# Kernel optimization log

Measured on AMD Instinct MI355X. Metric: run time of the kernel, lower is better.

Reference implementation:

```python
import jax, jax.numpy as jnp
import numpy as np


def _gru_dir(x_seq, h0, w_ih, w_hh, b_ih, b_hh, reverse):
    """Single-direction GRU over time (PyTorch gate math, gate order r,z,n).
    x_seq: [T,B,I], h0: [B,H], w_ih: [3H,I], w_hh: [3H,H].
    Returns outputs [T,B,H] in original time order."""
    # Precompute input projections for all timesteps in one GEMM.
    gi = jnp.einsum('tbi,gi->tbg', x_seq, w_ih) + b_ih  # [T,B,3H]

    def step(h, gi_t):
        gh = h @ w_hh.T + b_hh                     # [B,3H]
        ir, iz, inn = jnp.split(gi_t, 3, axis=-1)
        hr, hz, hn = jnp.split(gh, 3, axis=-1)
        r = jax.nn.sigmoid(ir + hr)
        z = jax.nn.sigmoid(iz + hz)
        n = jnp.tanh(inn + r * hn)
        h_new = (1.0 - z) * n + z * h
        return h_new, h_new

    _, ys = jax.lax.scan(step, h0, gi, reverse=reverse)
    return ys


def setup_inputs() -> dict:
    key = jax.random.key(0)
    ks = jax.random.split(key, 6)
    T, B, I, H, L = 256, 64, 2048, 1024, 3
    s = 1.0 / np.sqrt(H)  # PyTorch-style init scale
    return {
        'x': jax.random.normal(ks[0], (T, B, I), jnp.float32),
        'h0': jax.random.normal(ks[1], (2 * L, B, H), jnp.float32),
        'w_ih': jax.random.normal(ks[2], (L, 2, 3 * H, I), jnp.float32) * s,
        'w_hh': jax.random.normal(ks[3], (L, 2, 3 * H, H), jnp.float32) * s,
        'b_ih': jax.random.normal(ks[4], (L, 2, 3 * H), jnp.float32) * s,
        'b_hh': jax.random.normal(ks[5], (L, 2, 3 * H), jnp.float32) * s,
    }


def reference(x, h0, w_ih, w_hh, b_ih, b_hh):
    L = w_ih.shape[0]
    inp = x
    for l in range(L):  # small fixed layer loop
        yf = _gru_dir(inp, h0[2 * l], w_ih[l, 0], w_hh[l, 0], b_ih[l, 0], b_hh[l, 0], reverse=False)
        yb = _gru_dir(inp, h0[2 * l + 1], w_ih[l, 1], w_hh[l, 1], b_ih[l, 1], b_hh[l, 1], reverse=True)
        inp = jnp.concatenate([yf, yb], axis=-1)  # [T,B,2H]
    return inp
```

## Files before the change

kernel.cpp:

```cpp
#include <hip/hip_runtime.h>
#include <cstdint>

typedef __attribute__((ext_vector_type(8))) short short8;
typedef __attribute__((ext_vector_type(4))) float floatx4;
typedef __attribute__((ext_vector_type(2))) unsigned long long u64x2;

typedef unsigned short u16;
typedef unsigned int u32;
typedef unsigned long long u64;

template<int N> struct IC { static constexpr int v = N; };

__device__ __forceinline__ u16 f2bf(float x) {
    u32 u = __builtin_bit_cast(u32, x);
    u32 r = (u + 0x7fffu + ((u >> 16) & 1u)) >> 16;
    return (u16)r;
}
__device__ __forceinline__ float bf2f(u16 u) {
    return __builtin_bit_cast(float, (u32)u << 16);
}

__device__ __forceinline__ void gload_lds16(const void* g, void* l) {
    __builtin_amdgcn_global_load_lds(
        (const __attribute__((address_space(1))) void*)g,
        (__attribute__((address_space(3))) void*)l, 16, 0, 0);
}

__global__ __launch_bounds__(256) void cvt_f32_bf16(const float* __restrict__ src,
                                                    u16* __restrict__ dst, long n) {
    long i = ((long)blockIdx.x * 256 + threadIdx.x) * 8;
    if (i >= n) return;
    float4 a = *(const float4*)(src + i);
    float4 b = *(const float4*)(src + i + 4);
    short8 o;
    o[0] = (short)f2bf(a.x); o[1] = (short)f2bf(a.y);
    o[2] = (short)f2bf(a.z); o[3] = (short)f2bf(a.w);
    o[4] = (short)f2bf(b.x); o[5] = (short)f2bf(b.y);
    o[6] = (short)f2bf(b.z); o[7] = (short)f2bf(b.w);
    *(short8*)(dst + i) = o;
}

__global__ __launch_bounds__(256) void h_init(const float* __restrict__ h0,
                                              u16* __restrict__ H16G, int layer) {
    int idx = blockIdx.x * 256 + threadIdx.x;
    int d = idx >> 16;
    int r = idx & 65535;
    int b = r >> 10;
    int j = r & 1023;
    float v = h0[(long)(2 * layer + d) * 65536 + r];
    H16G[(long)(0 * 8 + d * 4 + (b >> 4)) * 16384 + (b & 15) * 1024 + j] = f2bf(v);
}

__global__ void zero_sync(int* s) {
    __hip_atomic_store(&s[blockIdx.x * 512 + threadIdx.x], 0,
                       __ATOMIC_RELAXED, __HIP_MEMORY_SCOPE_AGENT);
}

template<int BLOCKED_A>
__global__ __launch_bounds__(256) void gemm_bt_bf16(const u16* __restrict__ A,
                                                    const u16* __restrict__ B,
                                                    u16* __restrict__ C) {
    __shared__ u16 As[128 * 64];
    __shared__ u16 Bs[128 * 64];
    const int tid = threadIdx.x;
    const int w = tid >> 6, l = tid & 63;
    const int m0 = blockIdx.y * 128;
    const int n0 = blockIdx.x * 128;
    const int wr = w >> 1, wc = w & 1;

    floatx4 acc[4][4] = {};

    const int lr = tid >> 3;
    const int ch = tid & 7;
    long bA[4];
#pragma unroll
    for (int c = 0; c < 4; ++c) {
        const int m = m0 + lr + 32 * c;
        if (BLOCKED_A)
            bA[c] = (long)(ch >> 1) * 262144 + (m >> 6) * 1024 + (m & 63) * 16 + (ch & 1) * 8;
        else
            bA[c] = (long)m * 2048 + ch * 8;
    }
    const long kstride = BLOCKED_A ? 1048576 : 64;
    const u16* gB = B + (long)(n0 + lr) * 2048 + ch * 8;

    for (int kt = 0; kt < 32; ++kt) {
#pragma unroll
        for (int c = 0; c < 4; ++c)
            gload_lds16(A + bA[c] + kt * kstride, &As[c * 2048 + tid * 8]);
#pragma unroll
        for (int c = 0; c < 4; ++c)
            gload_lds16(gB + (long)c * 65536 + kt * 64, &Bs[c * 2048 + tid * 8]);
        __syncthreads();
#pragma unroll
        for (int ks = 0; ks < 2; ++ks) {
            short8 af[4], bfr[4];
#pragma unroll
            for (int mt = 0; mt < 4; ++mt)
                af[mt] = *(const short8*)&As[(wr * 64 + mt * 16 + (l & 15)) * 64 + ks * 32 + (l >> 4) * 8];
#pragma unroll
            for (int nt = 0; nt < 4; ++nt)
                bfr[nt] = *(const short8*)&Bs[(wc * 64 + nt * 16 + (l & 15)) * 64 + ks * 32 + (l >> 4) * 8];
#pragma unroll
            for (int mt = 0; mt < 4; ++mt)
#pragma unroll
                for (int nt = 0; nt < 4; ++nt)
                    acc[mt][nt] = __builtin_amdgcn_mfma_f32_16x16x32_bf16(af[mt], bfr[nt], acc[mt][nt], 0, 0, 0);
        }
        __syncthreads();
    }
    const int t_row = blockIdx.y * 2 + wr;
#pragma unroll
    for (int nt = 0; nt < 4; ++nt) {
        const int col = n0 + wc * 64 + nt * 16 + (l & 15);
        const int dir = col / 3072;
        const int rem = col - dir * 3072;
        const int gate = rem >> 10;
        const int j = rem & 1023;
        const int base = (((dir * 64 + (j >> 4)) * 256 + t_row) * 64) * 48 + gate * 16 + (j & 15);
#pragma unroll
        for (int mt = 0; mt < 4; ++mt)
#pragma unroll
            for (int i = 0; i < 4; ++i) {
                const int b = mt * 16 + (l >> 4) * 4 + i;
                C[base + b * 48] = f2bf(acc[mt][nt][i]);
            }
    }
}

__global__ __launch_bounds__(512, 1) void gru_scan(const u16* __restrict__ WHH,
                                                   const u16* __restrict__ GIn,
                                                   const float* __restrict__ bih,
                                                   const float* __restrict__ bhh,
                                                   const float* __restrict__ h0l,
                                                   u16* H16G,
                                                   u16* Ybf,
                                                   float* Yf32,
                                                   int* flags) {
    __shared__ float P[2][4][4][3][16][20];
    __shared__ int sh_role, sh_fast;
    const int tid = threadIdx.x;

    int* ctl = flags + 8192;
    if (tid == 0) {
        u32 xcc;
        asm volatile("s_getreg_b32 %0, hwreg(HW_REG_XCC_ID)" : "=s"(xcc));
        xcc &= 7u;
        int r = __hip_atomic_fetch_add(&ctl[(int)xcc], 1, __ATOMIC_RELAXED, __HIP_MEMORY_SCOPE_AGENT);
        int role = (r < 32) ? ((int)xcc * 32 + r) : -1;
        __hip_atomic_fetch_add(&ctl[8], 1, __ATOMIC_ACQ_REL, __HIP_MEMORY_SCOPE_AGENT);
        while (__hip_atomic_load(&ctl[8], __ATOMIC_ACQUIRE, __HIP_MEMORY_SCOPE_AGENT) < 256)
            __builtin_amdgcn_s_sleep(8);
        if (role < 0) {
            int f[8];
            for (int x = 0; x < 8; ++x) {
                int v = __hip_atomic_load(&ctl[x], __ATOMIC_RELAXED, __HIP_MEMORY_SCOPE_AGENT);
                f[x] = v > 32 ? 32 : v;
            }
            int r2 = __hip_atomic_fetch_add(&ctl[9], 1, __ATOMIC_RELAXED, __HIP_MEMORY_SCOPE_AGENT);
            int cum = 0;
            for (int x = 0; x < 8; ++x) {
                const int d = 32 - f[x];
                if (role < 0 && r2 < cum + d) role = x * 32 + f[x] + (r2 - cum);
                cum += d;
            }
        }
        const int g = role >> 5;
        __hip_atomic_store(&ctl[32 + role], (int)xcc, __ATOMIC_RELAXED, __HIP_MEMORY_SCOPE_AGENT);
        __hip_atomic_fetch_add(&ctl[16 + g], 1, __ATOMIC_ACQ_REL, __HIP_MEMORY_SCOPE_AGENT);
        while (__hip_atomic_load(&ctl[16 + g], __ATOMIC_ACQUIRE, __HIP_MEMORY_SCOPE_AGENT) < 32)
            __builtin_amdgcn_s_sleep(8);
        int fast = 1;
        for (int k = 0; k < 32; ++k)
            if (__hip_atomic_load(&ctl[32 + g * 32 + k], __ATOMIC_RELAXED, __HIP_MEMORY_SCOPE_AGENT) != (int)xcc)
                fast = 0;
        sh_role = role;
        sh_fast = fast;
    }
    __syncthreads();
    const int role = sh_role;
    const int fastv = sh_fast;

    const int w = tid >> 6, l = tid & 63;
    const int jg = w >> 2;
    const int kw = w & 3;
    const int g = role >> 5;
    const int jc = role & 31;
    const int dir = g >> 2;
    const int bh = g & 3;
    const int lrow = l & 15;
    const int lhi = l >> 4;

    int* gflags = flags + g * 1024;

    const u16* wbase = WHH + (long)dir * 3072 * 1024;
    short8 breg[3][8];
#pragma unroll
    for (int nt = 0; nt < 3; ++nt) {
        const long row = nt * 1024 + jc * 32 + jg * 16 + lrow;
#pragma unroll
        for (int kk = 0; kk < 8; ++kk)
            breg[nt][kk] = *(const short8*)&wbase[row * 1024 + (kw * 8 + kk) * 32 + lhi * 8];
    }

    const int jd = jc * 32 + jg * 16 + lrow;
    const int jb = jc * 2 + jg;
    const float bihR = bih[dir * 3072 + jd];
    const float bihZ = bih[dir * 3072 + 1024 + jd];
    const float bihN = bih[dir * 3072 + 2048 + jd];
    const float bhhR = bhh[dir * 3072 + jd];
    const float bhhZ = bhh[dir * 3072 + 1024 + jd];
    const float bhhN = bhh[dir * 3072 + 2048 + jd];

    const int b_loc = kw * 4 + lhi;
    const int b_glob = bh * 16 + b_loc;
    float hreg = h0l[dir * 65536 + b_glob * 1024 + jd];

    const u16* gib = GIn + (long)(dir * 64 + jb) * 256 * 3072 + b_glob * 48 + lrow;

    u16 givR, givZ, givN;
    {
        const long toff = (long)(dir ? 255 : 0) * 3072;
        givR = __builtin_nontemporal_load(gib + toff);
        givZ = __builtin_nontemporal_load(gib + toff + 16);
        givN = __builtin_nontemporal_load(gib + toff + 32);
    }

#define LOADH(DST, KK)                                                          \
        {                                                                       \
            const u16* p = hb16 + lrow * 1024 + kw * 256 + (KK) * 32 + lhi * 8; \
            if constexpr (FAST) {                                               \
                DST = *(const short8*)p;                                        \
            } else {                                                            \
                const u64* q8 = (const u64*)p;                                  \
                u64x2 q;                                                        \
                q[0] = __hip_atomic_load(q8,     __ATOMIC_RELAXED, __HIP_MEMORY_SCOPE_AGENT); \
                q[1] = __hip_atomic_load(q8 + 1, __ATOMIC_RELAXED, __HIP_MEMORY_SCOPE_AGENT); \
                DST = __builtin_bit_cast(short8, q);                            \
            }                                                                   \
        }
#define MFMA3(SRC, KK)                                                          \
        {                                                                       \
            _Pragma("unroll")                                                   \
            for (int nt = 0; nt < 3; ++nt)                                      \
                acc[nt] = __builtin_amdgcn_mfma_f32_16x16x32_bf16(              \
                    SRC, breg[nt][KK], acc[nt], 0, 0, 0);                       \
        }

    auto body = [&](auto fc) {
        constexpr int FAST = decltype(fc)::v;
        for (int s = 0; s < 256; ++s) {
            const int parity = s & 1;
            const int t_eff = dir ? (255 - s) : s;
            if constexpr (FAST) {
                asm volatile("buffer_inv sc0" ::: "memory");
            }
            const u16* hb16 = H16G + (long)(parity * 8 + g) * 16384;

            short8 afX, afY, afZ, afW;
            floatx4 acc[3] = {};
            LOADH(afX, 0)
            LOADH(afY, 1)
            LOADH(afZ, 2)
            LOADH(afW, 3)
            MFMA3(afX, 0) LOADH(afX, 4)
            MFMA3(afY, 1) LOADH(afY, 5)
            MFMA3(afZ, 2) LOADH(afZ, 6)
            MFMA3(afW, 3) LOADH(afW, 7)
            MFMA3(afX, 4)
            MFMA3(afY, 5)
            MFMA3(afZ, 6)
            MFMA3(afW, 7)

#pragma unroll
            for (int nt = 0; nt < 3; ++nt)
                *(floatx4*)&P[jg][kw][0][nt][lrow][lhi * 4] = acc[nt];
            asm volatile("s_waitcnt lgkmcnt(0)" ::: "memory");
            __builtin_amdgcn_sched_barrier(0);
            __builtin_amdgcn_s_barrier();
            __builtin_amdgcn_sched_barrier(0);

            float sR = 0.f, sZ = 0.f, sN = 0.f;
#pragma unroll
            for (int wp = 0; wp < 4; ++wp) {
                sR += P[jg][wp][0][0][lrow][b_loc];
                sZ += P[jg][wp][0][1][lrow][b_loc];
                sN += P[jg][wp][0][2][lrow][b_loc];
            }
            const float xr = bf2f(givR) + bihR + sR + bhhR;
            const float xz = bf2f(givZ) + bihZ + sZ + bhhZ;
            const float rg = 1.f / (1.f + __expf(-xr));
            const float zg = 1.f / (1.f + __expf(-xz));
            float xn = bf2f(givN) + bihN + rg * (sN + bhhN);
            xn = fminf(fmaxf(xn, -20.f), 20.f);
            const float e2 = __expf(-2.f * xn);
            const float ng = (1.f - e2) / (1.f + e2);
            const float hnew = (1.f - zg) * ng + zg * hreg;
            hreg = hnew;

            __builtin_amdgcn_sched_barrier(0);
            {
                u16* hp = H16G + (long)((parity ^ 1) * 8 + g) * 16384 + b_loc * 1024 + jd;
                if constexpr (FAST) *hp = f2bf(hnew);
                else __hip_atomic_store(hp, f2bf(hnew), __ATOMIC_RELAXED, __HIP_MEMORY_SCOPE_AGENT);
            }
            __builtin_amdgcn_sched_barrier(0);
            if (Yf32) {
                __builtin_nontemporal_store(hnew,
                    Yf32 + (long)(t_eff * 64 + b_glob) * 2048 + dir * 1024 + jd);
            } else {
                __builtin_nontemporal_store(f2bf(hnew),
                    Ybf + ((long)(dir * 64 + jb) * 256 + t_eff) * 1024 + b_glob * 16 + lrow);
            }
            __builtin_amdgcn_sched_barrier(0);
            asm volatile("s_waitcnt vmcnt(1)" ::: "memory");
            __builtin_amdgcn_sched_barrier(0);
            __builtin_amdgcn_s_barrier();
            if (tid == 0) {
                if constexpr (FAST) ((volatile int*)gflags)[jc * 32] = s + 1;
                else __hip_atomic_store(&gflags[jc * 32], s + 1, __ATOMIC_RELAXED, __HIP_MEMORY_SCOPE_AGENT);
            }

            u16 gnR = 0, gnZ = 0, gnN = 0;
            if (s < 255) {
                const long toff = (long)(dir ? (254 - s) : (s + 1)) * 3072;
                gnR = __builtin_nontemporal_load(gib + toff);
                gnZ = __builtin_nontemporal_load(gib + toff + 16);
                gnN = __builtin_nontemporal_load(gib + toff + 32);
            }

            if (w == 0) {
                if constexpr (FAST) {
                    while (true) {
                        asm volatile("buffer_inv sc0" ::: "memory");
                        int v = ((volatile int*)gflags)[(l & 31) * 32];
                        if (v >= s + 1) break;
                        __builtin_amdgcn_s_sleep(1);
                    }
                } else {
                    while (__hip_atomic_load(&gflags[(l & 31) * 32], __ATOMIC_RELAXED, __HIP_MEMORY_SCOPE_AGENT) < s + 1)
                        __builtin_amdgcn_s_sleep(1);
                }
            }
            __builtin_amdgcn_sched_barrier(0);
            __builtin_amdgcn_s_barrier();
            __builtin_amdgcn_sched_barrier(0);

            givR = gnR; givZ = gnZ; givN = gnN;
        }
    };
    if (fastv) body(IC<1>{});
    else       body(IC<0>{});
#undef LOADH
#undef MFMA3
}

extern "C" void kernel_launch(void* const* d_in, const int* in_sizes, int n_in,
                              void* d_out, int out_size, void* d_ws, size_t ws_size,
                              hipStream_t stream) {
    const float* x    = (const float*)d_in[0];
    const float* h0   = (const float*)d_in[1];
    const float* w_ih = (const float*)d_in[2];
    const float* w_hh = (const float*)d_in[3];
    const float* b_ih = (const float*)d_in[4];
    const float* b_hh = (const float*)d_in[5];
    float* out = (float*)d_out;

    char* ws = (char*)d_ws;
    u16*   XB0 = (u16*)(ws);
    u16*   XB1 = (u16*)(ws + 67108864);
    u16*   GI  = (u16*)(ws + 134217728);
    u16*   WIH = (u16*)(ws + 335544320);
    u16*   WHH = (u16*)(ws + 360710144);
    u16*   H16 = (u16*)(ws + 374341632);
    int*   SYNC = (int*)WIH;

    cvt_f32_bf16<<<16384, 256, 0, stream>>>(x, XB0, 33554432L);

    for (int layer = 0; layer < 3; ++layer) {
        const u16* xin = (layer == 1) ? XB1 : XB0;
        u16* yout = (layer == 0) ? XB1 : ((layer == 1) ? XB0 : nullptr);

        cvt_f32_bf16<<<6144, 256, 0, stream>>>(w_ih + (long)layer * 12582912, WIH, 12582912L);
        cvt_f32_bf16<<<3072, 256, 0, stream>>>(w_hh + (long)layer * 6291456, WHH, 6291456L);
        h_init<<<512, 256, 0, stream>>>(h0, H16, layer);

        dim3 g(48, 128);
        if (layer == 0)
            gemm_bt_bf16<0><<<g, 256, 0, stream>>>(xin, WIH, GI);
        else
            gemm_bt_bf16<1><<<g, 256, 0, stream>>>(xin, WIH, GI);

        zero_sync<<<17, 512, 0, stream>>>(SYNC);

        const float* bihl = b_ih + (long)layer * 6144;
        const float* bhhl = b_hh + (long)layer * 6144;
        gru_scan<<<256, 512, 0, stream>>>(WHH, GI, bihl, bhhl,
                                          h0 + (long)(2 * layer) * 65536, H16,
                                          yout, (layer == 2) ? out : nullptr, SYNC);
    }
}
```

Baseline: 4.008 ms.

## Replace block barriers with per-wave flag sync and double-buffer partial sums

Result: slower. 8.913 ms (+122.4%).

```diff
diff --git a/kernel.cpp b/kernel.cpp
--- a/kernel.cpp
+++ b/kernel.cpp
@@ -137,11 +137,12 @@
                                                    u16* Ybf,
                                                    float* Yf32,
                                                    int* flags) {
-    __shared__ float P[2][4][4][3][16][20];
+    __shared__ float P[2][2][4][3][16][20];
+    __shared__ float lds_pad[5248];
     __shared__ int sh_role, sh_fast;
     const int tid = threadIdx.x;
 
-    int* ctl = flags + 8192;
+    int* ctl = flags + 2048;
     if (tid == 0) {
         u32 xcc;
         asm volatile("s_getreg_b32 %0, hwreg(HW_REG_XCC_ID)" : "=s"(xcc));
@@ -180,6 +181,7 @@
     __syncthreads();
     const int role = sh_role;
     const int fastv = sh_fast;
+    if (fastv == 2) ((volatile float*)lds_pad)[tid] = 0.f;
 
     const int w = tid >> 6, l = tid & 63;
     const int jg = w >> 2;
@@ -191,7 +193,8 @@
     const int lrow = l & 15;
     const int lhi = l >> 4;
 
-    int* gflags = flags + g * 1024;
+    int* gflags = flags + g * 256;
+    const int slot = jc * 8 + w;
 
     const u16* wbase = WHH + (long)dir * 3072 * 1024;
     short8 breg[3][8];
@@ -263,6 +266,15 @@
             LOADH(afY, 1)
             LOADH(afZ, 2)
             LOADH(afW, 3)
+
+            u16 gnR = 0, gnZ = 0, gnN = 0;
+            if (s < 255) {
+                const long toff = (long)(dir ? (254 - s) : (s + 1)) * 3072;
+                gnR = __builtin_nontemporal_load(gib + toff);
+                gnZ = __builtin_nontemporal_load(gib + toff + 16);
+                gnN = __builtin_nontemporal_load(gib + toff + 32);
+            }
+
             MFMA3(afX, 0) LOADH(afX, 4)
             MFMA3(afY, 1) LOADH(afY, 5)
             MFMA3(afZ, 2) LOADH(afZ, 6)
@@ -274,7 +286,7 @@
 
 #pragma unroll
             for (int nt = 0; nt < 3; ++nt)
-                *(floatx4*)&P[jg][kw][0][nt][lrow][lhi * 4] = acc[nt];
+                *(floatx4*)&P[parity][jg][kw][nt][lrow][lhi * 4] = acc[nt];
             asm volatile("s_waitcnt lgkmcnt(0)" ::: "memory");
             __builtin_amdgcn_sched_barrier(0);
             __builtin_amdgcn_s_barrier();
@@ -283,9 +295,9 @@
             float sR = 0.f, sZ = 0.f, sN = 0.f;
 #pragma unroll
             for (int wp = 0; wp < 4; ++wp) {
-                sR += P[jg][wp][0][0][lrow][b_loc];
-                sZ += P[jg][wp][0][1][lrow][b_loc];
-                sN += P[jg][wp][0][2][lrow][b_loc];
+                sR += P[parity][jg][wp][0][lrow][b_loc];
+                sZ += P[parity][jg][wp][1][lrow][b_loc];
+                sN += P[parity][jg][wp][2][lrow][b_loc];
             }
             const float xr = bf2f(givR) + bihR + sR + bhhR;
             const float xz = bf2f(givZ) + bihZ + sZ + bhhZ;
@@ -304,47 +316,36 @@
                 if constexpr (FAST) *hp = f2bf(hnew);
                 else __hip_atomic_store(hp, f2bf(hnew), __ATOMIC_RELAXED, __HIP_MEMORY_SCOPE_AGENT);
             }
+            if (Yf32) {
+                Yf32[(long)(t_eff * 64 + b_glob) * 2048 + dir * 1024 + jd] = hnew;
+            } else {
+                Ybf[((long)(dir * 64 + jb) * 256 + t_eff) * 1024 + b_glob * 16 + lrow] = f2bf(hnew);
+            }
             __builtin_amdgcn_sched_barrier(0);
-            if (Yf32) {
-                __builtin_nontemporal_store(hnew,
-                    Yf32 + (long)(t_eff * 64 + b_glob) * 2048 + dir * 1024 + jd);
+            asm volatile("s_waitcnt vmcnt(0)" ::: "memory");
+            __builtin_amdgcn_sched_barrier(0);
+
+            if constexpr (FAST) {
+                if (l == 0) ((volatile int*)gflags)[slot] = s + 1;
+                while (true) {
+                    asm volatile("buffer_inv sc0" ::: "memory");
+                    const volatile int* f4 = (const volatile int*)gflags;
+                    int a = f4[l * 4], b = f4[l * 4 + 1], c = f4[l * 4 + 2], d = f4[l * 4 + 3];
+                    if (__all(a >= s + 1 && b >= s + 1 && c >= s + 1 && d >= s + 1)) break;
+                    __builtin_amdgcn_s_sleep(1);
+                }
             } else {
-                __builtin_nontemporal_store(f2bf(hnew),
-                    Ybf + ((long)(dir * 64 + jb) * 256 + t_eff) * 1024 + b_glob * 16 + lrow);
-            }
-            __builtin_amdgcn_sched_barrier(0);
-            asm volatile("s_waitcnt vmcnt(1)" ::: "memory");
-            __builtin_amdgcn_sched_barrier(0);
-            __builtin_amdgcn_s_barrier();
-            if (tid == 0) {
-                if constexpr (FAST) ((volatile int*)gflags)[jc * 32] = s + 1;
-                else __hip_atomic_store(&gflags[jc * 32], s + 1, __ATOMIC_RELAXED, __HIP_MEMORY_SCOPE_AGENT);
-            }
-
-            u16 gnR = 0, gnZ = 0, gnN = 0;
-            if (s < 255) {
-                const long toff = (long)(dir ? (254 - s) : (s + 1)) * 3072;
-                gnR = __builtin_nontemporal_load(gib + toff);
-                gnZ = __builtin_nontemporal_load(gib + toff + 16);
-                gnN = __builtin_nontemporal_load(gib + toff + 32);
-            }
-
-            if (w == 0) {
-                if constexpr (FAST) {
-                    while (true) {
-                        asm volatile("buffer_inv sc0" ::: "memory");
-                        int v = ((volatile int*)gflags)[(l & 31) * 32];
-                        if (v >= s + 1) break;
-                        __builtin_amdgcn_s_sleep(1);
-                    }
-                } else {
-                    while (__hip_atomic_load(&gflags[(l & 31) * 32], __ATOMIC_RELAXED, __HIP_MEMORY_SCOPE_AGENT) < s + 1)
-                        __builtin_amdgcn_s_sleep(1);
+                if (l == 0)
+                    __hip_atomic_store(&gflags[slot], s + 1, __ATOMIC_RELAXED, __HIP_MEMORY_SCOPE_AGENT);
+                while (true) {
+                    int a = __hip_atomic_load(&gflags[l * 4],     __ATOMIC_RELAXED, __HIP_MEMORY_SCOPE_AGENT);
+                    int b = __hip_atomic_load(&gflags[l * 4 + 1], __ATOMIC_RELAXED, __HIP_MEMORY_SCOPE_AGENT);
+                    int c = __hip_atomic_load(&gflags[l * 4 + 2], __ATOMIC_RELAXED, __HIP_MEMORY_SCOPE_AGENT);
+                    int d = __hip_atomic_load(&gflags[l * 4 + 3], __ATOMIC_RELAXED, __HIP_MEMORY_SCOPE_AGENT);
+                    if (__all(a >= s + 1 && b >= s + 1 && c >= s + 1 && d >= s + 1)) break;
+                    __builtin_amdgcn_s_sleep(1);
                 }
             }
-            __builtin_amdgcn_sched_barrier(0);
-            __builtin_amdgcn_s_barrier();
-            __builtin_amdgcn_sched_barrier(0);
 
             givR = gnR; givZ = gnZ; givN = gnN;
         }
@@ -391,7 +392,7 @@
         else
             gemm_bt_bf16<1><<<g, 256, 0, stream>>>(xin, WIH, GI);
 
-        zero_sync<<<17, 512, 0, stream>>>(SYNC);
+        zero_sync<<<5, 512, 0, stream>>>(SYNC);
 
         const float* bihl = b_ih + (long)layer * 6144;
         const float* bhhl = b_hh + (long)layer * 6144;
```
